# Optimization experiments

Hardware: AMD Instinct MI355X
Metric: run time of the kernel (lower is better)

The kernel has to match this reference:

```python
import jax, jax.numpy as jnp
import numpy as np

N_TIME = 512          # n_time_nodes
LATENT = 32           # latent_dim
HIDDEN = 64           # hidden_dim
N_MODES = 8           # r_fourier_modes
X_A0 = 0.3            # initial stoichiometry (anode)
CSANMAX = 28700.0     # max concentration scale
BASE_LOGIT = float(np.log(X_A0 / (1.0 - X_A0)))  # logit_from_fraction(x_a0)
FEAT_DIM = 1 + 2 * N_MODES   # [rho, cos(k*pi*rho), sin(k*pi*rho)]
IN_DIM = LATENT + FEAT_DIM
N_POINTS = 2_000_000


def setup_inputs() -> dict:
    key = jax.random.key(0)
    ks = jax.random.split(key, 8)
    time_idx = jax.random.randint(ks[0], (N_POINTS,), 0, N_TIME)
    rho = jax.random.uniform(ks[1], (N_POINTS,), dtype=jnp.float32)
    # trainable latent code per nonzero time node
    emb = jax.random.normal(ks[2], (N_TIME - 1, LATENT), dtype=jnp.float32) * 0.02
    # decoder_a: Linear(IN,HID)+SiLU, Linear(HID,HID)+SiLU, Linear(HID,1)
    W0 = jax.random.normal(ks[3], (IN_DIM, HIDDEN), dtype=jnp.float32) / np.sqrt(IN_DIM)
    b0 = jnp.zeros((HIDDEN,), jnp.float32)
    W1 = jax.random.normal(ks[4], (HIDDEN, HIDDEN), dtype=jnp.float32) / np.sqrt(HIDDEN)
    b1 = jnp.zeros((HIDDEN,), jnp.float32)
    Wout = jax.random.normal(ks[5], (HIDDEN, 1), dtype=jnp.float32) * 0.1
    bout = jnp.zeros((1,), jnp.float32)
    return {"time_idx": time_idx, "rho": rho, "emb": emb,
            "W0": W0, "b0": b0, "W1": W1, "b1": b1, "Wout": Wout, "bout": bout}


def _radius_features(rho):
    # [N] -> [N, 1 + 2*N_MODES]
    k = jnp.arange(1, N_MODES + 1, dtype=rho.dtype)
    ang = jnp.pi * rho[:, None] * k[None, :]
    return jnp.concatenate([rho[:, None], jnp.cos(ang), jnp.sin(ang)], axis=1)


def reference(time_idx, rho, emb, W0, b0, W1, b1, Wout, bout):
    # predicated version of the torch masked scatter: compute everywhere,
    # select initial-condition value where time_idx == 0
    idx = jnp.clip(time_idx - 1, 0, N_TIME - 2)       # safe gather index
    e = emb[idx]                                       # [N, LATENT]
    feat = _radius_features(rho)                       # [N, FEAT_DIM]
    h = jnp.concatenate([e, feat], axis=1)             # [N, IN_DIM]
    h = jax.nn.silu(h @ W0 + b0)
    h = jax.nn.silu(h @ W1 + b1)
    raw = (h @ Wout + bout)[:, 0]                      # [N]
    theta = jax.nn.sigmoid(raw + BASE_LOGIT)
    return jnp.where(time_idx == 0, X_A0 * CSANMAX, theta * CSANMAX)
```

## Files before the change

### kernel.cpp

```cpp
#include <hip/hip_runtime.h>
#include <stdint.h>


typedef _Float16 half8  __attribute__((ext_vector_type(8)));
typedef _Float16 half4v __attribute__((ext_vector_type(4)));
typedef _Float16 half2v __attribute__((ext_vector_type(2)));
typedef float f32x4 __attribute__((ext_vector_type(4)));

#define LOG2E 1.44269504088896340736f
#define NLN2  -0.6931471805599453f
#define CSCL  -1.44269504088896340736f
#define BASE_LOGIT -0.84729786038720367f
#define CSANMAX 28700.0f
#define IC_VAL 8610.0f

__device__ __forceinline__ float fast_exp2(float x) { return __builtin_amdgcn_exp2f(x); }
__device__ __forceinline__ float fast_rcp(float x)  { return __builtin_amdgcn_rcpf(x); }
__device__ __forceinline__ void usilu2(float u0, float u1, float& p0, float& p1) {
  const float d0 = 1.0f + fast_exp2(u0);
  const float d1 = 1.0f + fast_exp2(u1);
  const float r  = fast_rcp(d0 * d1);
  p0 = u0 * d1 * r;
  p1 = u1 * d0 * r;
}
__device__ __forceinline__ half2v pkh(float a, float b) {
  return __builtin_bit_cast(half2v, __builtin_amdgcn_cvt_pkrtz(a, b));
}

union H8 { half8 v8; half2v v2[4]; half4v v4[2]; };
union H4 { half4v v4; half2v v2[2]; };

__global__ __launch_bounds__(256, 3) void mlp_kernel(
    const int* __restrict__ tix, const float* __restrict__ rho,
    const float* __restrict__ emb, const float* __restrict__ W0,
    const float* __restrict__ b0, const float* __restrict__ W1,
    const float* __restrict__ b1, const float* __restrict__ Wout,
    const float* __restrict__ bout, float* __restrict__ out, int ntiles)
{
  __shared__ __align__(16) _Float16 stage[2][2][4][64][8];

  const int tid  = threadIdx.x;
  const int wid  = tid >> 6;
  const int lane = tid & 63;
  const int m    = lane & 15;
  const int q    = lane >> 4;

  if (wid == 0) {
#pragma unroll
    for (int t = 0; t < 4; ++t) {
#pragma unroll
      for (int s = 0; s < 2; ++s) {
        half8 f0, f1;
#pragma unroll
        for (int j = 0; j < 8; ++j) {
          const int k = s * 32 + q * 8 + j;
          const int n = t * 16 + m;
          float v0;
          if (k < 32) {
            v0 = W0[k * 64 + n];
          } else {
            const int kn = k - 32;
            v0 = (kn < 16) ? W0[(33 + kn) * 64 + n]
               : (kn == 16) ? W0[32 * 64 + n]
               : (kn == 17) ? b0[n] : 0.0f;
          }
          f0[j] = (_Float16)(CSCL * v0);
          const int hm = (s * 2 + (j >> 2)) * 16 + q * 4 + (j & 3);
          f1[j] = (_Float16)W1[hm * 64 + n];
        }
        *(half8*)&stage[0][s][t][lane][0] = f0;
        *(half8*)&stage[1][s][t][lane][0] = f1;
      }
    }
  }

  half2v biash[8];
  half2v wouth[8];
#pragma unroll
  for (int t = 0; t < 4; ++t) {
    const f32x4 bv = *(const f32x4*)(b1 + t * 16 + q * 4);
    const f32x4 wv = *(const f32x4*)(Wout + t * 16 + q * 4);
    biash[t * 2]     = pkh(CSCL * bv[0], CSCL * bv[1]);
    biash[t * 2 + 1] = pkh(CSCL * bv[2], CSCL * bv[3]);
    wouth[t * 2]     = pkh(NLN2 * wv[0], NLN2 * wv[1]);
    wouth[t * 2 + 1] = pkh(NLN2 * wv[2], NLN2 * wv[3]);
  }
  const float boutBL = bout[0] + BASE_LOGIT;

  __syncthreads();

  half8 w0A[4], w0B[4], w1A[4], w1B[4];
#pragma unroll
  for (int t = 0; t < 4; ++t) {
    w0A[t] = *(const half8*)&stage[0][0][t][lane][0];
    w0B[t] = *(const half8*)&stage[0][1][t][lane][0];
    w1A[t] = *(const half8*)&stage[1][0][t][lane][0];
    w1B[t] = *(const half8*)&stage[1][1][t][lane][0];
  }

  const f32x4 z = {0.0f, 0.0f, 0.0f, 0.0f};
  const int S = gridDim.x * 4;

  int tg = blockIdx.x * 4 + wid;
  if (tg >= ntiles) return;
  const int lim = ntiles - 1;

  int   tC = tix[tg * 16 + m];
  float rC = rho[tg * 16 + m];
  const int tg1 = min(tg + S, lim);
  int   tN = tix[tg1 * 16 + m];
  float rN = rho[tg1 * 16 + m];
  H8 X0C;
  {
    const int idx = min(max(tC - 1, 0), 510);
    const float* e = emb + (size_t)idx * 32 + q * 8;
    const f32x4 e0 = *(const f32x4*)e;
    const f32x4 e1 = *(const f32x4*)(e + 4);
    X0C.v2[0] = pkh(e0[0], e0[1]); X0C.v2[1] = pkh(e0[2], e0[3]);
    X0C.v2[2] = pkh(e1[0], e1[1]); X0C.v2[3] = pkh(e1[2], e1[3]);
  }

  while (true) {
    const int tg2 = min(tg + 2 * S, lim);
    const int   tQ = tix[tg2 * 16 + m];
    const float rQ = rho[tg2 * 16 + m];
    const int idxN = min(max(tN - 1, 0), 510);
    const float* ern = emb + (size_t)idxN * 32 + q * 8;
    const f32x4 eN0 = *(const f32x4*)ern;
    const f32x4 eN1 = *(const f32x4*)(ern + 4);

    const float rev = 0.5f * rC;
    const float c1  = __builtin_amdgcn_cosf(rev);
    const float s1f = __builtin_amdgcn_sinf(rev);
    const float tc  = 2.0f * c1;
    const float x1v = (q == 0) ? c1 : ((q == 1) ? s1f : 0.0f);
    const float x0v = (q == 0) ? 1.0f : 0.0f;
    const float x2v = tc * x1v - x0v;
    const float x3v = tc * x2v - x1v;
    const float x4v = tc * x3v - x2v;
    const float x5v = tc * x4v - x3v;
    const float x6v = tc * x5v - x4v;
    const float x7v = tc * x6v - x5v;
    const float x8v = tc * x7v - x6v;
    H8 X1;
    X1.v2[0] = (q == 2) ? pkh(rC, 1.0f) : pkh(x1v, x2v);
    X1.v2[1] = pkh(x3v, x4v);
    X1.v2[2] = pkh(x5v, x6v);
    X1.v2[3] = pkh(x7v, x8v);

    f32x4 acc[4];
#pragma unroll
    for (int t = 0; t < 4; ++t) {
      f32x4 a = __builtin_amdgcn_mfma_f32_16x16x32_f16(w0A[t], X0C.v8, z, 0, 0, 0);
      a = __builtin_amdgcn_mfma_f32_16x16x32_f16(w0B[t], X1.v8, a, 0, 0, 0);
      acc[t] = a;
    }
    H4 hh[4];
#pragma unroll
    for (int t = 0; t < 4; ++t) {
      float p0, p1, p2, p3;
      usilu2(acc[t][0], acc[t][1], p0, p1);
      usilu2(acc[t][2], acc[t][3], p2, p3);
      hh[t].v2[0] = pkh(p0, p1);
      hh[t].v2[1] = pkh(p2, p3);
    }
    H8 Y0, Y1;
    Y0.v4[0] = hh[0].v4; Y0.v4[1] = hh[1].v4;
    Y1.v4[0] = hh[2].v4; Y1.v4[1] = hh[3].v4;

#pragma unroll
    for (int t = 0; t < 4; ++t) {
      f32x4 a = __builtin_amdgcn_mfma_f32_16x16x32_f16(w1A[t], Y0.v8, z, 0, 0, 0);
      a = __builtin_amdgcn_mfma_f32_16x16x32_f16(w1B[t], Y1.v8, a, 0, 0, 0);
      acc[t] = a;
    }
    float dA = 0.0f, dB = 0.0f;
#pragma unroll
    for (int t = 0; t < 4; ++t) {
      float p0, p1, p2, p3;
      const float u0 = (float)biash[t * 2][0]     + acc[t][0];
      const float u1 = (float)biash[t * 2][1]     + acc[t][1];
      const float u2 = (float)biash[t * 2 + 1][0] + acc[t][2];
      const float u3 = (float)biash[t * 2 + 1][1] + acc[t][3];
      usilu2(u0, u1, p0, p1);
      usilu2(u2, u3, p2, p3);
      dA = fmaf(p0, (float)wouth[t * 2][0],     dA);
      dB = fmaf(p1, (float)wouth[t * 2][1],     dB);
      dA = fmaf(p2, (float)wouth[t * 2 + 1][0], dA);
      dB = fmaf(p3, (float)wouth[t * 2 + 1][1], dB);
    }
    float dot = dA + dB;
    dot += __shfl_xor(dot, 16, 64);
    dot += __shfl_xor(dot, 32, 64);

    const float theta = fast_rcp(1.0f + fast_exp2(-LOG2E * (dot + boutBL)));
    const float val = (tC == 0) ? IC_VAL : theta * CSANMAX;
    if (q == 0) out[tg * 16 + m] = val;

    const int tgn = tg + S;
    if (tgn >= ntiles) break;
    tg = tgn;
    X0C.v2[0] = pkh(eN0[0], eN0[1]); X0C.v2[1] = pkh(eN0[2], eN0[3]);
    X0C.v2[2] = pkh(eN1[0], eN1[1]); X0C.v2[3] = pkh(eN1[2], eN1[3]);
    tC = tN; rC = rN;
    tN = tQ; rN = rQ;
  }
}

extern "C" void kernel_launch(void* const* d_in, const int* in_sizes, int n_in,
                              void* d_out, int out_size, void* d_ws, size_t ws_size,
                              hipStream_t stream) {
  const int*   tix  = (const int*)d_in[0];
  const float* rho  = (const float*)d_in[1];
  const float* emb  = (const float*)d_in[2];
  const float* W0   = (const float*)d_in[3];
  const float* b0   = (const float*)d_in[4];
  const float* W1   = (const float*)d_in[5];
  const float* b1   = (const float*)d_in[6];
  const float* Wout = (const float*)d_in[7];
  const float* bout = (const float*)d_in[8];
  float* outp = (float*)d_out;

  const int n      = in_sizes[0];
  const int ntiles = n / 16;

  int grid = 1024;
  const int maxg = (ntiles + 3) / 4;
  if (grid > maxg) grid = maxg;
  mlp_kernel<<<dim3(grid), dim3(256), 0, stream>>>(
      tix, rho, emb, W0, b0, W1, b1, Wout, bout, outp, ntiles);
}
```

Measured before the change: 168.0 us.

## Software-pipeline MLP layers across tiles to overlap layer-1 and layer-2 work

Splits each tile's work into two phases (first-layer MFMA plus SiLU, then second-layer MFMA, SiLU, output dot and store). The loop now runs phase 2 of the previous tile alongside phase 1 of the current tile, with a prologue and epilogue. This removes the serial dependency between the two layers inside one iteration so MFMA and transcendental VALU work from independent tiles can interleave. It costs extra live registers for the carried Y0/Y1 fragments, which may hurt occupancy at launch bounds of 3 waves.

```diff
diff --git a/kernel.cpp b/kernel.cpp
--- a/kernel.cpp
+++ b/kernel.cpp
@@ -105,6 +105,77 @@
   if (tg >= ntiles) return;
   const int lim = ntiles - 1;
 
+  auto phase1 = [&](float rhp, half8 X0v, H8& Y0o, H8& Y1o) {
+    const float rev = 0.5f * rhp;
+    const float c1  = __builtin_amdgcn_cosf(rev);
+    const float s1f = __builtin_amdgcn_sinf(rev);
+    const float tc  = 2.0f * c1;
+    const float x1v = (q == 0) ? c1 : ((q == 1) ? s1f : 0.0f);
+    const float x0v = (q == 0) ? 1.0f : 0.0f;
+    const float x2v = tc * x1v - x0v;
+    const float x3v = tc * x2v - x1v;
+    const float x4v = tc * x3v - x2v;
+    const float x5v = tc * x4v - x3v;
+    const float x6v = tc * x5v - x4v;
+    const float x7v = tc * x6v - x5v;
+    const float x8v = tc * x7v - x6v;
+    H8 X1;
+    X1.v2[0] = (q == 2) ? pkh(rhp, 1.0f) : pkh(x1v, x2v);
+    X1.v2[1] = pkh(x3v, x4v);
+    X1.v2[2] = pkh(x5v, x6v);
+    X1.v2[3] = pkh(x7v, x8v);
+
+    f32x4 acc[4];
+#pragma unroll
+    for (int t = 0; t < 4; ++t) {
+      f32x4 a = __builtin_amdgcn_mfma_f32_16x16x32_f16(w0A[t], X0v, z, 0, 0, 0);
+      a = __builtin_amdgcn_mfma_f32_16x16x32_f16(w0B[t], X1.v8, a, 0, 0, 0);
+      acc[t] = a;
+    }
+    H4 hh[4];
+#pragma unroll
+    for (int t = 0; t < 4; ++t) {
+      float p0, p1, p2, p3;
+      usilu2(acc[t][0], acc[t][1], p0, p1);
+      usilu2(acc[t][2], acc[t][3], p2, p3);
+      hh[t].v2[0] = pkh(p0, p1);
+      hh[t].v2[1] = pkh(p2, p3);
+    }
+    Y0o.v4[0] = hh[0].v4; Y0o.v4[1] = hh[1].v4;
+    Y1o.v4[0] = hh[2].v4; Y1o.v4[1] = hh[3].v4;
+  };
+
+  auto phase2 = [&](const H8& Y0p, const H8& Y1p, int icP, int tgP) {
+    f32x4 acc[4];
+#pragma unroll
+    for (int t = 0; t < 4; ++t) {
+      f32x4 a = __builtin_amdgcn_mfma_f32_16x16x32_f16(w1A[t], Y0p.v8, z, 0, 0, 0);
+      a = __builtin_amdgcn_mfma_f32_16x16x32_f16(w1B[t], Y1p.v8, a, 0, 0, 0);
+      acc[t] = a;
+    }
+    float dA = 0.0f, dB = 0.0f;
+#pragma unroll
+    for (int t = 0; t < 4; ++t) {
+      float p0, p1, p2, p3;
+      const float u0 = (float)biash[t * 2][0]     + acc[t][0];
+      const float u1 = (float)biash[t * 2][1]     + acc[t][1];
+      const float u2 = (float)biash[t * 2 + 1][0] + acc[t][2];
+      const float u3 = (float)biash[t * 2 + 1][1] + acc[t][3];
+      usilu2(u0, u1, p0, p1);
+      usilu2(u2, u3, p2, p3);
+      dA = fmaf(p0, (float)wouth[t * 2][0],     dA);
+      dB = fmaf(p1, (float)wouth[t * 2][1],     dB);
+      dA = fmaf(p2, (float)wouth[t * 2 + 1][0], dA);
+      dB = fmaf(p3, (float)wouth[t * 2 + 1][1], dB);
+    }
+    float dot = dA + dB;
+    dot += __shfl_xor(dot, 16, 64);
+    dot += __shfl_xor(dot, 32, 64);
+    const float theta = fast_rcp(1.0f + fast_exp2(-LOG2E * (dot + boutBL)));
+    const float val = (icP == 0) ? IC_VAL : theta * CSANMAX;
+    if (q == 0) out[tgP * 16 + m] = val;
+  };
+
   int   tC = tix[tg * 16 + m];
   float rC = rho[tg * 16 + m];
   const int tg1 = min(tg + S, lim);
@@ -119,8 +190,26 @@
     X0C.v2[0] = pkh(e0[0], e0[1]); X0C.v2[1] = pkh(e0[2], e0[3]);
     X0C.v2[2] = pkh(e1[0], e1[1]); X0C.v2[3] = pkh(e1[2], e1[3]);
   }
-
-  while (true) {
+  H8 Y0p, Y1p;
+  phase1(rC, X0C.v8, Y0p, Y1p);
+  int icP = tC, tgP = tg;
+  {
+    const int idx = min(max(tN - 1, 0), 510);
+    const float* e = emb + (size_t)idx * 32 + q * 8;
+    const f32x4 e0 = *(const f32x4*)e;
+    const f32x4 e1 = *(const f32x4*)(e + 4);
+    X0C.v2[0] = pkh(e0[0], e0[1]); X0C.v2[1] = pkh(e0[2], e0[3]);
+    X0C.v2[2] = pkh(e1[0], e1[1]); X0C.v2[3] = pkh(e1[2], e1[3]);
+  }
+  tC = tN; rC = rN;
+  {
+    const int tg2 = min(tg + 2 * S, lim);
+    tN = tix[tg2 * 16 + m];
+    rN = rho[tg2 * 16 + m];
+  }
+  tg += S;
+
+  while (tg < ntiles) {
     const int tg2 = min(tg + 2 * S, lim);
     const int   tQ = tix[tg2 * 16 + m];
     const float rQ = rho[tg2 * 16 + m];
@@ -129,82 +218,18 @@
     const f32x4 eN0 = *(const f32x4*)ern;
     const f32x4 eN1 = *(const f32x4*)(ern + 4);
 
-    const float rev = 0.5f * rC;
-    const float c1  = __builtin_amdgcn_cosf(rev);
-    const float s1f = __builtin_amdgcn_sinf(rev);
-    const float tc  = 2.0f * c1;
-    const float x1v = (q == 0) ? c1 : ((q == 1) ? s1f : 0.0f);
-    const float x0v = (q == 0) ? 1.0f : 0.0f;
-    const float x2v = tc * x1v - x0v;
-    const float x3v = tc * x2v - x1v;
-    const float x4v = tc * x3v - x2v;
-    const float x5v = tc * x4v - x3v;
-    const float x6v = tc * x5v - x4v;
-    const float x7v = tc * x6v - x5v;
-    const float x8v = tc * x7v - x6v;
-    H8 X1;
-    X1.v2[0] = (q == 2) ? pkh(rC, 1.0f) : pkh(x1v, x2v);
-    X1.v2[1] = pkh(x3v, x4v);
-    X1.v2[2] = pkh(x5v, x6v);
-    X1.v2[3] = pkh(x7v, x8v);
-
-    f32x4 acc[4];
-#pragma unroll
-    for (int t = 0; t < 4; ++t) {
-      f32x4 a = __builtin_amdgcn_mfma_f32_16x16x32_f16(w0A[t], X0C.v8, z, 0, 0, 0);
-      a = __builtin_amdgcn_mfma_f32_16x16x32_f16(w0B[t], X1.v8, a, 0, 0, 0);
-      acc[t] = a;
-    }
-    H4 hh[4];
-#pragma unroll
-    for (int t = 0; t < 4; ++t) {
-      float p0, p1, p2, p3;
-      usilu2(acc[t][0], acc[t][1], p0, p1);
-      usilu2(acc[t][2], acc[t][3], p2, p3);
-      hh[t].v2[0] = pkh(p0, p1);
-      hh[t].v2[1] = pkh(p2, p3);
-    }
-    H8 Y0, Y1;
-    Y0.v4[0] = hh[0].v4; Y0.v4[1] = hh[1].v4;
-    Y1.v4[0] = hh[2].v4; Y1.v4[1] = hh[3].v4;
-
-#pragma unroll
-    for (int t = 0; t < 4; ++t) {
-      f32x4 a = __builtin_amdgcn_mfma_f32_16x16x32_f16(w1A[t], Y0.v8, z, 0, 0, 0);
-      a = __builtin_amdgcn_mfma_f32_16x16x32_f16(w1B[t], Y1.v8, a, 0, 0, 0);
-      acc[t] = a;
-    }
-    float dA = 0.0f, dB = 0.0f;
-#pragma unroll
-    for (int t = 0; t < 4; ++t) {
-      float p0, p1, p2, p3;
-      const float u0 = (float)biash[t * 2][0]     + acc[t][0];
-      const float u1 = (float)biash[t * 2][1]     + acc[t][1];
-      const float u2 = (float)biash[t * 2 + 1][0] + acc[t][2];
-      const float u3 = (float)biash[t * 2 + 1][1] + acc[t][3];
-      usilu2(u0, u1, p0, p1);
-      usilu2(u2, u3, p2, p3);
-      dA = fmaf(p0, (float)wouth[t * 2][0],     dA);
-      dB = fmaf(p1, (float)wouth[t * 2][1],     dB);
-      dA = fmaf(p2, (float)wouth[t * 2 + 1][0], dA);
-      dB = fmaf(p3, (float)wouth[t * 2 + 1][1], dB);
-    }
-    float dot = dA + dB;
-    dot += __shfl_xor(dot, 16, 64);
-    dot += __shfl_xor(dot, 32, 64);
-
-    const float theta = fast_rcp(1.0f + fast_exp2(-LOG2E * (dot + boutBL)));
-    const float val = (tC == 0) ? IC_VAL : theta * CSANMAX;
-    if (q == 0) out[tg * 16 + m] = val;
-
-    const int tgn = tg + S;
-    if (tgn >= ntiles) break;
-    tg = tgn;
+    phase2(Y0p, Y1p, icP, tgP);
+    phase1(rC, X0C.v8, Y0p, Y1p);
+
+    icP = tC; tgP = tg;
     X0C.v2[0] = pkh(eN0[0], eN0[1]); X0C.v2[1] = pkh(eN0[2], eN0[3]);
     X0C.v2[2] = pkh(eN1[0], eN1[1]); X0C.v2[3] = pkh(eN1[2], eN1[3]);
     tC = tN; rC = rN;
     tN = tQ; rN = rQ;
-  }
+    tg += S;
+  }
+
+  phase2(Y0p, Y1p, icP, tgP);
 }
 
 extern "C" void kernel_launch(void* const* d_in, const int* in_sizes, int n_in,
```

Result: faster. 163.0 us (-3.0%).
